# Kernel optimization log

Hardware: AMD Instinct MI355X
Metric: run time of the kernel (lower is better)

## Reference

```python
import jax, jax.numpy as jnp
import numpy as np

# MalConv-style dims: byte vocab, tiny embed, wide stride-=kernel gated conv
B, T, V, E, C, K, S, N = 8, 1048576, 257, 8, 128, 512, 512, 64


def setup_inputs() -> dict:
    key = jax.random.key(0)
    k1, k2, k3, k4 = jax.random.split(key, 4)
    x = jax.random.randint(k1, (B, T), 0, V, dtype=jnp.int32)
    emb = jax.random.normal(k2, (V, E), dtype=jnp.float32) * 0.02
    fan = 1.0 / np.sqrt(E * K)
    w1 = jax.random.normal(k3, (C, E, K), dtype=jnp.float32) * fan
    w2 = jax.random.normal(k4, (C, E, K), dtype=jnp.float32) * fan
    b1 = jnp.zeros((C,), jnp.float32)
    b2 = jnp.zeros((C,), jnp.float32)
    return {"x": x, "emb": emb, "w1": w1, "b1": b1, "w2": w2, "b2": b2}


def reference(x, emb, w1, b1, w2, b2):
    # preprocess: byte embedding -> (B, E, T)
    z = emb[x].transpose(0, 2, 1)
    dn = ("NCH", "OIH", "NCH")
    # GatedConvolution: c1 * sigmoid(c2), valid conv, stride S -> (B, C, L)
    c1 = jax.lax.conv_general_dilated(z, w1, (S,), "VALID", dimension_numbers=dn) + b1[None, :, None]
    c2 = jax.lax.conv_general_dilated(z, w2, (S,), "VALID", dimension_numbers=dn) + b2[None, :, None]
    g = c1 * jax.nn.sigmoid(c2)  # (B, C, L)
    L = g.shape[-1]
    # input-space position of each conv output window; patch assignment
    pos = jnp.arange(L, dtype=jnp.int32) * S
    patch_size = -(-T // N)  # ceil(T / num_patches)
    seg = jnp.clip(pos // patch_size, 0, N - 1)  # (L,)
    # per-patch max-over-time, per channel: segment_max over the L axis
    gl = g.transpose(2, 0, 1).reshape(L, B * C)  # (L, B*C)
    mv = jax.ops.segment_max(gl, seg, num_segments=N)  # (N, B*C)
    max_vals = mv.reshape(N, B, C).transpose(1, 0, 2)  # (B, N, C)
    return max_vals
```

## Files before the change

kernel.cpp:

```cpp
#include <hip/hip_runtime.h>
#include <hip/hip_bf16.h>
#include <math.h>

#define M_TOT   16384
#define N_TOT   256
#define K_TOT   4096

typedef __bf16 bf16x8 __attribute__((ext_vector_type(8)));
typedef float  f32x4  __attribute__((ext_vector_type(4)));

#define WS_WP_OFF   0
#define WS_EMB_OFF  (2u << 20)
#define WS_C_OFF    (4u << 20)

__device__ __forceinline__ void load_lds16(const void* g, void* l) {
    __builtin_amdgcn_global_load_lds(
        (const __attribute__((address_space(1))) void*)g,
        (__attribute__((address_space(3))) void*)l,
        16, 0, 0);
}

__global__ void prep_kernel(const float* __restrict__ w1,
                            const float* __restrict__ w2,
                            const float* __restrict__ emb,
                            __bf16* __restrict__ Wp,
                            __bf16* __restrict__ embp) {
    int bid = blockIdx.x;
    if (bid < 4096) {
        int u  = bid * 256 + (int)threadIdx.x;
        int e  = u & 7;
        int n  = (u >> 3) & 63;
        int q  = (u >> 9) & 3;
        int t  = (u >> 11) & 7;
        int s  = (u >> 14) & 15;
        int nt = u >> 18;
        int c  = (nt << 6) | n;
        int byte = (s << 5) | (q << 3) | t;
        float v;
        if (c < 128) v = w1[(c << 12) + (e << 9) + byte];
        else         v = w2[((c - 128) << 12) + (e << 9) + byte];
        Wp[u] = (__bf16)v;
    } else {
        for (int i = threadIdx.x; i < 2056; i += 256)
            embp[i] = (__bf16)emb[i];
    }
}

__global__ __launch_bounds__(256, 2)
void gemm_kernel(const int* __restrict__ x,
                 const __bf16* __restrict__ Wp,
                 const uint4* __restrict__ embp,
                 float* __restrict__ Cbuf) {
    __shared__ uint4 ldsB[2048];
    __shared__ uint4 embl[260];

    const int tid  = threadIdx.x;
    const int wave = tid >> 6;
    const int lane = tid & 63;
    const int q    = lane >> 4;
    const int nl   = lane & 15;

    for (int i = tid; i < 257; i += 256) embl[i] = embp[i];

    const int nt = blockIdx.x & 3;
    const int mt = blockIdx.x >> 2;
    const int m0 = mt << 7;

    const int rowA0 = m0 + (wave << 5) + nl;
    const long xbase0 = (long)rowA0 * 512 + (q << 3);
    const long xbase1 = xbase0 + 16 * 512;

    const char* WpBase = (const char*)Wp + ((size_t)nt << 15) * 16;

    f32x4 acc[2][4] = {};

    for (int s = 0; s < 16; ++s) {
        const int* xp0 = x + xbase0 + (s << 5);
        const int* xp1 = x + xbase1 + (s << 5);
        int4 i0a = *(const int4*)xp0;
        int4 i0b = *(const int4*)(xp0 + 4);
        int4 i1a = *(const int4*)xp1;
        int4 i1b = *(const int4*)(xp1 + 4);

        {
            const char* src = WpBase + ((size_t)s << 15) + tid * 16;
            char* dst = (char*)ldsB + tid * 16;
#pragma unroll
            for (int i = 0; i < 8; ++i)
                load_lds16(src + i * 4096, dst + i * 4096);
        }
        __syncthreads();

        int idx0[8] = {i0a.x, i0a.y, i0a.z, i0a.w, i0b.x, i0b.y, i0b.z, i0b.w};
        int idx1[8] = {i1a.x, i1a.y, i1a.z, i1a.w, i1b.x, i1b.y, i1b.z, i1b.w};

#pragma unroll
        for (int t = 0; t < 8; ++t) {
            bf16x8 a0 = *reinterpret_cast<const bf16x8*>(&embl[idx0[t]]);
            bf16x8 a1 = *reinterpret_cast<const bf16x8*>(&embl[idx1[t]]);
#pragma unroll
            for (int nf = 0; nf < 4; ++nf) {
                bf16x8 b = *reinterpret_cast<const bf16x8*>(
                    (const char*)ldsB + (t << 12) + (q << 10) + (nf << 8) + (nl << 4));
                acc[0][nf] = __builtin_amdgcn_mfma_f32_16x16x32_bf16(a0, b, acc[0][nf], 0, 0, 0);
                acc[1][nf] = __builtin_amdgcn_mfma_f32_16x16x32_bf16(a1, b, acc[1][nf], 0, 0, 0);
            }
        }
        __syncthreads();
    }

#pragma unroll
    for (int rg = 0; rg < 2; ++rg) {
        int rowbase = m0 + (wave << 5) + (rg << 4) + (q << 2);
#pragma unroll
        for (int nf = 0; nf < 4; ++nf) {
            int col = (nt << 6) + (nf << 4) + nl;
#pragma unroll
            for (int i = 0; i < 4; ++i)
                Cbuf[(size_t)(rowbase + i) * 256 + col] = acc[rg][nf][i];
        }
    }
}

__global__ void reduce_kernel(const float* __restrict__ Cbuf,
                              const float* __restrict__ b1,
                              const float* __restrict__ b2,
                              float* __restrict__ out) {
    int tid  = threadIdx.x;
    int c    = tid & 127;
    int gp   = blockIdx.x * 2 + (tid >> 7);
    long mbase = (long)gp << 5;
    float bb1 = b1[c], bb2 = b2[c];
    float best = -INFINITY;
    const float* rowp = Cbuf + mbase * 256 + c;
#pragma unroll 4
    for (int l = 0; l < 32; ++l) {
        float c1 = rowp[0]   + bb1;
        float c2 = rowp[128] + bb2;
        float g  = c1 * (1.0f / (1.0f + __expf(-c2)));
        best = fmaxf(best, g);
        rowp += 256;
    }
    out[(size_t)gp * 128 + c] = best;
}

extern "C" void kernel_launch(void* const* d_in, const int* in_sizes, int n_in,
                              void* d_out, int out_size, void* d_ws, size_t ws_size,
                              hipStream_t stream) {
    const int*   x   = (const int*)d_in[0];
    const float* emb = (const float*)d_in[1];
    const float* w1  = (const float*)d_in[2];
    const float* b1  = (const float*)d_in[3];
    const float* w2  = (const float*)d_in[4];
    const float* b2  = (const float*)d_in[5];
    float* out = (float*)d_out;

    char* ws = (char*)d_ws;
    __bf16* Wp    = (__bf16*)(ws + WS_WP_OFF);
    __bf16* embp  = (__bf16*)(ws + WS_EMB_OFF);
    float*  Cbuf  = (float*)(ws + WS_C_OFF);

    prep_kernel<<<4097, 256, 0, stream>>>(w1, w2, emb, Wp, embp);
    gemm_kernel<<<512, 256, 0, stream>>>(x, Wp, (const uint4*)embp, Cbuf);
    reduce_kernel<<<256, 256, 0, stream>>>(Cbuf, b1, b2, out);
}
```

Baseline: 128.0 us.

## Double-buffer weight tiles, enlarge M tile, add split-K, coalesce weight prep

```diff
diff --git a/kernel.cpp b/kernel.cpp
--- a/kernel.cpp
+++ b/kernel.cpp
@@ -2,9 +2,6 @@
 #include <hip/hip_bf16.h>
 #include <math.h>
 
-#define M_TOT   16384
-#define N_TOT   256
-#define K_TOT   4096
 
 typedef __bf16 bf16x8 __attribute__((ext_vector_type(8)));
 typedef float  f32x4  __attribute__((ext_vector_type(4)));
@@ -23,26 +20,44 @@
 __global__ void prep_kernel(const float* __restrict__ w1,
                             const float* __restrict__ w2,
                             const float* __restrict__ emb,
-                            __bf16* __restrict__ Wp,
+                            uint4* __restrict__ Wp4,
                             __bf16* __restrict__ embp) {
     int bid = blockIdx.x;
-    if (bid < 4096) {
-        int u  = bid * 256 + (int)threadIdx.x;
-        int e  = u & 7;
-        int n  = (u >> 3) & 63;
-        int q  = (u >> 9) & 3;
-        int t  = (u >> 11) & 7;
-        int s  = (u >> 14) & 15;
-        int nt = u >> 18;
-        int c  = (nt << 6) | n;
-        int byte = (s << 5) | (q << 3) | t;
-        float v;
-        if (c < 128) v = w1[(c << 12) + (e << 9) + byte];
-        else         v = w2[((c - 128) << 12) + (e << 9) + byte];
-        Wp[u] = (__bf16)v;
+    int tid = threadIdx.x;
+    if (bid < 128) {
+        __shared__ __bf16 lds[8192];
+        int cb = bid & 7;
+        int sB = bid >> 3;
+        int c0 = cb << 5;
+        const float* wsrc = (c0 < 128) ? (w1 + ((size_t)c0 << 12))
+                                       : (w2 + ((size_t)(c0 - 128) << 12));
+        int j4  = tid & 7;
+        int pr0 = tid >> 3;
+#pragma unroll
+        for (int p = 0; p < 8; ++p) {
+            int pair = p * 32 + pr0;
+            int cl = pair >> 3, e = pair & 7;
+            const float4 v = *(const float4*)(wsrc + (cl << 12) + (e << 9) + (sB << 5) + (j4 << 2));
+            float vv[4] = {v.x, v.y, v.z, v.w};
+#pragma unroll
+            for (int jj = 0; jj < 4; ++jj) {
+                int j = (j4 << 2) + jj;
+                int qq = j >> 3, tt = j & 7;
+                lds[(((qq << 3) + tt) * 32 + cl) * 8 + e] = (__bf16)vv[jj];
+            }
+        }
+        __syncthreads();
+        const uint4* l4 = (const uint4*)lds;
+        int nhalf = cb & 1, nt = cb >> 1;
+        int base = (nt << 15) + (sB << 11) + (nhalf << 5);
+#pragma unroll
+        for (int it = 0; it < 4; ++it) {
+            int idx = it * 256 + tid;
+            int qq = idx >> 8, tt = (idx >> 5) & 7, w = idx & 31;
+            Wp4[base + (tt << 8) + (qq << 6) + w] = l4[idx];
+        }
     } else {
-        for (int i = threadIdx.x; i < 2056; i += 256)
-            embp[i] = (__bf16)emb[i];
+        for (int i = tid; i < 2056; i += 256) embp[i] = (__bf16)emb[i];
     }
 }
 
@@ -50,9 +65,10 @@
 void gemm_kernel(const int* __restrict__ x,
                  const __bf16* __restrict__ Wp,
                  const uint4* __restrict__ embp,
-                 float* __restrict__ Cbuf) {
-    __shared__ uint4 ldsB[2048];
-    __shared__ uint4 embl[260];
+                 float* __restrict__ Cbuf,
+                 int ksplit) {
+    __shared__ uint4 ldsB[2][2048];
+    __shared__ uint4 embl[257];
 
     const int tid  = threadIdx.x;
     const int wave = tid >> 6;
@@ -62,62 +78,96 @@
 
     for (int i = tid; i < 257; i += 256) embl[i] = embp[i];
 
-    const int nt = blockIdx.x & 3;
-    const int mt = blockIdx.x >> 2;
-    const int m0 = mt << 7;
-
-    const int rowA0 = m0 + (wave << 5) + nl;
-    const long xbase0 = (long)rowA0 * 512 + (q << 3);
-    const long xbase1 = xbase0 + 16 * 512;
-
-    const char* WpBase = (const char*)Wp + ((size_t)nt << 15) * 16;
-
-    f32x4 acc[2][4] = {};
-
-    for (int s = 0; s < 16; ++s) {
-        const int* xp0 = x + xbase0 + (s << 5);
-        const int* xp1 = x + xbase1 + (s << 5);
-        int4 i0a = *(const int4*)xp0;
-        int4 i0b = *(const int4*)(xp0 + 4);
-        int4 i1a = *(const int4*)xp1;
-        int4 i1b = *(const int4*)(xp1 + 4);
-
-        {
-            const char* src = WpBase + ((size_t)s << 15) + tid * 16;
-            char* dst = (char*)ldsB + tid * 16;
-#pragma unroll
-            for (int i = 0; i < 8; ++i)
-                load_lds16(src + i * 4096, dst + i * 4096);
+    const int bid = blockIdx.x;
+    int mt, nt, kh, nsteps, s0;
+    if (ksplit == 2) {
+        mt = ((bid >> 6) << 3) | (bid & 7);
+        int combo = (bid >> 3) & 7;
+        kh = combo & 1; nt = combo >> 1;
+        nsteps = 8; s0 = kh << 3;
+    } else {
+        mt = ((bid >> 5) << 3) | (bid & 7);
+        nt = (bid >> 3) & 3;
+        kh = 0; nsteps = 16; s0 = 0;
+    }
+    const int m0 = mt << 8;
+    const int rA = m0 + (wave << 6) + nl;
+    const char* WpBase = (const char*)Wp + ((size_t)nt << 19);
+
+    const int* xp[4];
+#pragma unroll
+    for (int rg = 0; rg < 4; ++rg)
+        xp[rg] = x + (size_t)(rA + (rg << 4)) * 512 + (q << 3);
+
+    int4 xc[4][2];
+#pragma unroll
+    for (int rg = 0; rg < 4; ++rg) {
+        const int* p = xp[rg] + (s0 << 5);
+        xc[rg][0] = *(const int4*)p;
+        xc[rg][1] = *(const int4*)(p + 4);
+    }
+    {
+        const char* src = WpBase + ((size_t)s0 << 15) + tid * 16;
+        char* dst = (char*)&ldsB[0][0] + tid * 16;
+#pragma unroll
+        for (int i = 0; i < 8; ++i) load_lds16(src + i * 4096, dst + i * 4096);
+    }
+    __syncthreads();
+
+    f32x4 acc[4][4] = {};
+
+    for (int ss = 0; ss < nsteps; ++ss) {
+        const int sp  = s0 + ss;
+        const int buf = ss & 1;
+        if (ss + 1 < nsteps) {
+            const char* src = WpBase + ((size_t)(sp + 1) << 15) + tid * 16;
+            char* dst = (char*)&ldsB[buf ^ 1][0] + tid * 16;
+#pragma unroll
+            for (int i = 0; i < 8; ++i) load_lds16(src + i * 4096, dst + i * 4096);
+        }
+        int idx[4][8];
+#pragma unroll
+        for (int rg = 0; rg < 4; ++rg) {
+            idx[rg][0] = xc[rg][0].x; idx[rg][1] = xc[rg][0].y;
+            idx[rg][2] = xc[rg][0].z; idx[rg][3] = xc[rg][0].w;
+            idx[rg][4] = xc[rg][1].x; idx[rg][5] = xc[rg][1].y;
+            idx[rg][6] = xc[rg][1].z; idx[rg][7] = xc[rg][1].w;
+        }
+        const int spn = (ss + 1 < nsteps) ? sp + 1 : sp;
+#pragma unroll
+        for (int rg = 0; rg < 4; ++rg) {
+            const int* p = xp[rg] + (spn << 5);
+            xc[rg][0] = *(const int4*)p;
+            xc[rg][1] = *(const int4*)(p + 4);
+        }
+        const char* Bbase = (const char*)&ldsB[buf][0] + (q << 10) + (nl << 4);
+#pragma unroll
+        for (int t = 0; t < 8; ++t) {
+            bf16x8 a[4];
+#pragma unroll
+            for (int rg = 0; rg < 4; ++rg)
+                a[rg] = *reinterpret_cast<const bf16x8*>(&embl[idx[rg][t]]);
+#pragma unroll
+            for (int nf = 0; nf < 4; ++nf) {
+                bf16x8 b = *reinterpret_cast<const bf16x8*>(Bbase + (t << 12) + (nf << 8));
+#pragma unroll
+                for (int rg = 0; rg < 4; ++rg)
+                    acc[rg][nf] = __builtin_amdgcn_mfma_f32_16x16x32_bf16(a[rg], b, acc[rg][nf], 0, 0, 0);
+            }
         }
         __syncthreads();
-
-        int idx0[8] = {i0a.x, i0a.y, i0a.z, i0a.w, i0b.x, i0b.y, i0b.z, i0b.w};
-        int idx1[8] = {i1a.x, i1a.y, i1a.z, i1a.w, i1b.x, i1b.y, i1b.z, i1b.w};
-
-#pragma unroll
-        for (int t = 0; t < 8; ++t) {
-            bf16x8 a0 = *reinterpret_cast<const bf16x8*>(&embl[idx0[t]]);
-            bf16x8 a1 = *reinterpret_cast<const bf16x8*>(&embl[idx1[t]]);
-#pragma unroll
-            for (int nf = 0; nf < 4; ++nf) {
-                bf16x8 b = *reinterpret_cast<const bf16x8*>(
-                    (const char*)ldsB + (t << 12) + (q << 10) + (nf << 8) + (nl << 4));
-                acc[0][nf] = __builtin_amdgcn_mfma_f32_16x16x32_bf16(a0, b, acc[0][nf], 0, 0, 0);
-                acc[1][nf] = __builtin_amdgcn_mfma_f32_16x16x32_bf16(a1, b, acc[1][nf], 0, 0, 0);
-            }
-        }
-        __syncthreads();
-    }
-
-#pragma unroll
-    for (int rg = 0; rg < 2; ++rg) {
-        int rowbase = m0 + (wave << 5) + (rg << 4) + (q << 2);
+    }
+
+    float* Cout = Cbuf + (size_t)kh * (16384 * 256);
+#pragma unroll
+    for (int rg = 0; rg < 4; ++rg) {
+        int rowb = m0 + (wave << 6) + (rg << 4) + (q << 2);
 #pragma unroll
         for (int nf = 0; nf < 4; ++nf) {
             int col = (nt << 6) + (nf << 4) + nl;
 #pragma unroll
             for (int i = 0; i < 4; ++i)
-                Cbuf[(size_t)(rowbase + i) * 256 + col] = acc[rg][nf][i];
+                Cout[(size_t)(rowb + i) * 256 + col] = acc[rg][nf][i];
         }
     }
 }
@@ -125,23 +175,30 @@
 __global__ void reduce_kernel(const float* __restrict__ Cbuf,
                               const float* __restrict__ b1,
                               const float* __restrict__ b2,
-                              float* __restrict__ out) {
-    int tid  = threadIdx.x;
-    int c    = tid & 127;
-    int gp   = blockIdx.x * 2 + (tid >> 7);
-    long mbase = (long)gp << 5;
+                              float* __restrict__ out,
+                              int ksplit) {
+    __shared__ float sm[256];
+    int tid = threadIdx.x;
+    int c   = tid & 127;
+    int lh  = tid >> 7;
+    int gp  = blockIdx.x;
     float bb1 = b1[c], bb2 = b2[c];
+    const float* base0 = Cbuf + (size_t)(gp * 32 + lh * 16) * 256 + c;
+    const float* base1 = base0 + (size_t)16384 * 256;
+    const bool ks2 = (ksplit == 2);
     float best = -INFINITY;
-    const float* rowp = Cbuf + mbase * 256 + c;
 #pragma unroll 4
-    for (int l = 0; l < 32; ++l) {
-        float c1 = rowp[0]   + bb1;
-        float c2 = rowp[128] + bb2;
-        float g  = c1 * (1.0f / (1.0f + __expf(-c2)));
+    for (int l = 0; l < 16; ++l) {
+        float c1 = base0[0]   + bb1;
+        float c2 = base0[128] + bb2;
+        if (ks2) { c1 += base1[0]; c2 += base1[128]; }
+        float g = c1 * (1.0f / (1.0f + __expf(-c2)));
         best = fmaxf(best, g);
-        rowp += 256;
-    }
-    out[(size_t)gp * 128 + c] = best;
+        base0 += 256; base1 += 256;
+    }
+    sm[tid] = best;
+    __syncthreads();
+    if (lh == 0) out[(size_t)gp * 128 + c] = fmaxf(sm[tid], sm[tid + 128]);
 }
 
 extern "C" void kernel_launch(void* const* d_in, const int* in_sizes, int n_in,
@@ -156,11 +213,14 @@
     float* out = (float*)d_out;
 
     char* ws = (char*)d_ws;
-    __bf16* Wp    = (__bf16*)(ws + WS_WP_OFF);
-    __bf16* embp  = (__bf16*)(ws + WS_EMB_OFF);
-    float*  Cbuf  = (float*)(ws + WS_C_OFF);
-
-    prep_kernel<<<4097, 256, 0, stream>>>(w1, w2, emb, Wp, embp);
-    gemm_kernel<<<512, 256, 0, stream>>>(x, Wp, (const uint4*)embp, Cbuf);
-    reduce_kernel<<<256, 256, 0, stream>>>(Cbuf, b1, b2, out);
-}
+    __bf16* Wp   = (__bf16*)(ws + WS_WP_OFF);
+    __bf16* embp = (__bf16*)(ws + WS_EMB_OFF);
+    float*  Cbuf = (float*)(ws + WS_C_OFF);
+
+    const size_t need2 = (size_t)(4u << 20) + 2ull * 16384 * 256 * 4;
+    int ksplit = (ws_size >= need2) ? 2 : 1;
+
+    prep_kernel<<<129, 256, 0, stream>>>(w1, w2, emb, (uint4*)Wp, embp);
+    gemm_kernel<<<256 * ksplit, 256, 0, stream>>>(x, Wp, (const uint4*)embp, Cbuf, ksplit);
+    reduce_kernel<<<512, 256, 0, stream>>>(Cbuf, b1, b2, out, ksplit);
+}
```

Result: faster. 124.0 us (-3.1%).
